# Optimization experiments

Measured on AMD Instinct MI355X. Metric: run time of the kernel, lower is better.

Reference implementation:

```python
import jax, jax.numpy as jnp
import numpy as np

B, T, D = 4, 2048, 1024

def layer_norm(x, gamma, bias):
    # NOTE: faithfully reproduces the source's (buggy) LN: x - mu/sqrt(var), unbiased var
    mu = jnp.mean(x, axis=-1, keepdims=True)
    var = jnp.var(x, axis=-1, ddof=1, keepdims=True)
    return (x - mu / jnp.sqrt(var)) * gamma + bias

def setup_inputs() -> dict:
    key = jax.random.key(0)
    ks = jax.random.split(key, 8)
    scale = 1.0 / np.sqrt(D)
    return {
        'x': jax.random.normal(ks[0], (B, T, D), dtype=jnp.float32),
        'gamma1': jnp.ones((D,), jnp.float32),
        'beta1': jnp.zeros((D,), jnp.float32),
        'w_q': jax.random.uniform(ks[1], (D, D), jnp.float32, -scale, scale),
        'w_k': jax.random.uniform(ks[2], (D, D), jnp.float32, -scale, scale),
        'w_v': jax.random.uniform(ks[3], (D, D), jnp.float32, -scale, scale),
        'gamma2': jnp.ones((D,), jnp.float32),
        'beta2': jnp.zeros((D,), jnp.float32),
        'W1': jax.random.uniform(ks[4], (D, D), jnp.float32, -scale, scale),
        'b1': jnp.zeros((D,), jnp.float32),
        'W2': jax.random.uniform(ks[5], (D, D), jnp.float32, -scale, scale),
        'b2': jnp.zeros((D,), jnp.float32),
    }

def reference(x, gamma1, beta1, w_q, w_k, w_v, gamma2, beta2, W1, b1, W2, b2):
    d_model = x.shape[-1]
    t = x.shape[1]
    h = layer_norm(x, gamma1, beta1)
    q = jnp.einsum('btk,kd->btd', h, w_q)
    k = jnp.einsum('btk,kd->btd', h, w_k)
    v = jnp.einsum('btk,kd->btd', h, w_v)
    scale = 1.0 / jnp.sqrt(jnp.asarray(d_model, x.dtype))
    causal = jnp.tril(jnp.ones((t, t), dtype=bool))
    mask = jnp.where(causal, 0.0, -jnp.inf).astype(x.dtype)
    scores = jnp.einsum('bqd,bkd->bqk', q, k) * scale + mask
    attn = jax.nn.softmax(scores, axis=-1)
    y = jnp.einsum('bqt,btd->bqd', attn, v) + x
    h2 = layer_norm(y, gamma2, beta2)
    out = jnp.maximum(h2 @ W1 + b1, 0.0) @ W2 + b2
    return out + y
```

## Files before the change

kernel.cpp:

```cpp
#include <hip/hip_runtime.h>
#include <hip/hip_bf16.h>
#include <math.h>

using bf16 = __hip_bfloat16;

static constexpr int Bn = 4;
static constexpr int Tn = 2048;
static constexpr int Dn = 1024;

typedef __attribute__((ext_vector_type(8))) short bf16x8;
typedef __attribute__((ext_vector_type(4))) float f32x4;

__device__ __forceinline__ float ldf(float v) { return v; }
__device__ __forceinline__ float ldf(bf16 v) { return __bfloat162float(v); }
__device__ __forceinline__ bf16 f2b(float v) { return __float2bfloat16(v); }
__device__ __forceinline__ float b2f(short s) {
    return __uint_as_float(((unsigned)(unsigned short)s) << 16);
}
__device__ __forceinline__ short f2bs(float v) {
    bf16 t = __float2bfloat16(v);
    return *reinterpret_cast<short*>(&t);
}

template <typename T> __device__ __forceinline__ T from_float(float v);
template <> __device__ __forceinline__ float from_float<float>(float v) { return v; }
template <> __device__ __forceinline__ bf16 from_float<bf16>(float v) { return f2b(v); }

__device__ __forceinline__ void load4(const float* p, float* v) {
    const float4 t = *(const float4*)p;
    v[0] = t.x; v[1] = t.y; v[2] = t.z; v[3] = t.w;
}
__device__ __forceinline__ void load4(const bf16* p, float* v) {
    const short4 t = *(const short4*)p;
    v[0] = b2f(t.x); v[1] = b2f(t.y); v[2] = b2f(t.z); v[3] = b2f(t.w);
}

__device__ __forceinline__ void async_copy16(const bf16* g, bf16* l) {
    __builtin_amdgcn_global_load_lds(
        (const __attribute__((address_space(1))) void*)g,
        (__attribute__((address_space(3))) void*)l,
        16, 0, 0);
}

template <int BN, int EPI, typename OutT, bool RELU>
__global__ __launch_bounds__(512, 2) void gemm8p(
    const bf16* __restrict__ A, const bf16* __restrict__ Bm,
    OutT* __restrict__ C, const float* __restrict__ bias,
    const bf16* __restrict__ res, bf16* __restrict__ vtp,
    int K, int lda, int ldb, int ldc)
{
    static_assert(EPI != 1 || BN == 128, "V-transpose epilogue needs BN=128");
    constexpr int BM = 256, BK = 32;
    constexpr int NT = BN / 64;
    constexpr int BUFE = (BM + BN) * BK;
    __shared__ __align__(16) bf16 smem[3 * BUFE];

    const int bm = blockIdx.x, bn = blockIdx.y;
    const int tid = threadIdx.x;
    const int wave = tid >> 6;
    const int lane = tid & 63;
    const int wm = wave >> 2;
    const int wn = wave & 3;
    const int lr = lane >> 2;
    const int lc = (lane & 3) * 8;
    const int arow = lane & 15;
    const int kq = (lane >> 4) * 8;

    const int NK = K / BK;

    const bf16* gA0 = A + (size_t)(bm * BM + wave * 16 + lr) * lda + lc;
    const bf16* gA1 = A + (size_t)(bm * BM + (wave + 8) * 16 + lr) * lda + lc;
    const bf16* gB0 = Bm + (size_t)(bn * BN + wave * 16 + lr) * ldb + lc;
    const bf16* gB1 = (BN == 256)
        ? Bm + (size_t)(bn * BN + (wave + 8) * 16 + lr) * ldb + lc : nullptr;

    f32x4 acc[8][NT] = {};

    {
        bf16* As0 = smem;
        bf16* Bs0 = smem + BM * BK;
        bf16* As1 = smem + BUFE;
        bf16* Bs1 = smem + BUFE + BM * BK;
        async_copy16(gA0, As0 + wave * 512);
        async_copy16(gA1, As0 + (wave + 8) * 512);
        async_copy16(gB0, Bs0 + wave * 512);
        if constexpr (BN == 256) async_copy16(gB1, Bs0 + (wave + 8) * 512);
        async_copy16(gA0 + BK, As1 + wave * 512);
        async_copy16(gA1 + BK, As1 + (wave + 8) * 512);
        async_copy16(gB0 + BK, Bs1 + wave * 512);
        if constexpr (BN == 256) async_copy16(gB1 + BK, Bs1 + (wave + 8) * 512);
    }
    if constexpr (BN == 256) asm volatile("s_waitcnt vmcnt(4)" ::: "memory");
    else                     asm volatile("s_waitcnt vmcnt(3)" ::: "memory");
    __builtin_amdgcn_s_barrier();

    int cb = 0;
    int sb = 2;
    for (int kt = 0; kt < NK; ++kt) {
        const bf16* As = smem + cb * BUFE;
        const bf16* Bs = As + BM * BK;
        const bool st = (kt + 2) < NK;
        const int koff = (kt + 2) * BK;

        bf16x8 af[8], bf0[NT / 2];
#pragma unroll
        for (int mt = 0; mt < 8; ++mt)
            af[mt] = *(const bf16x8*)&As[(wm * 8 + mt) * 512 + arow * 32 + kq];
#pragma unroll
        for (int nt = 0; nt < NT / 2; ++nt)
            bf0[nt] = *(const bf16x8*)&Bs[(wn * NT + nt) * 512 + arow * 32 + kq];
        if (st) {
            bf16* Ad = smem + sb * BUFE;
            async_copy16(gA0 + koff, Ad + wave * 512);
            async_copy16(gA1 + koff, Ad + (wave + 8) * 512);
        }
        __builtin_amdgcn_s_barrier();
        asm volatile("s_waitcnt lgkmcnt(0)" ::: "memory");
        __builtin_amdgcn_sched_barrier(0);
        __builtin_amdgcn_s_setprio(1);
#pragma unroll
        for (int mt = 0; mt < 8; ++mt)
#pragma unroll
            for (int nt = 0; nt < NT / 2; ++nt)
                acc[mt][nt] = __builtin_amdgcn_mfma_f32_16x16x32_bf16(
                    af[mt], bf0[nt], acc[mt][nt], 0, 0, 0);
        __builtin_amdgcn_s_setprio(0);
        __builtin_amdgcn_s_barrier();

        bf16x8 bf1[NT / 2];
#pragma unroll
        for (int nt = 0; nt < NT / 2; ++nt)
            bf1[nt] = *(const bf16x8*)&Bs[(wn * NT + NT / 2 + nt) * 512 + arow * 32 + kq];
        if (st) {
            bf16* Bd = smem + sb * BUFE + BM * BK;
            async_copy16(gB0 + koff, Bd + wave * 512);
            if constexpr (BN == 256) async_copy16(gB1 + koff, Bd + (wave + 8) * 512);
        }
        __builtin_amdgcn_s_barrier();
        asm volatile("s_waitcnt lgkmcnt(0)" ::: "memory");
        __builtin_amdgcn_sched_barrier(0);
        __builtin_amdgcn_s_setprio(1);
#pragma unroll
        for (int mt = 0; mt < 8; ++mt)
#pragma unroll
            for (int nt = 0; nt < NT / 2; ++nt)
                acc[mt][NT / 2 + nt] = __builtin_amdgcn_mfma_f32_16x16x32_bf16(
                    af[mt], bf1[nt], acc[mt][NT / 2 + nt], 0, 0, 0);
        __builtin_amdgcn_s_setprio(0);
        if (st) {
            if constexpr (BN == 256) asm volatile("s_waitcnt vmcnt(4)" ::: "memory");
            else                     asm volatile("s_waitcnt vmcnt(3)" ::: "memory");
        } else {
            asm volatile("s_waitcnt vmcnt(0)" ::: "memory");
        }
        __builtin_amdgcn_s_barrier();

        cb = (cb + 1 == 3) ? 0 : cb + 1;
        sb = (sb + 1 == 3) ? 0 : sb + 1;
    }

    const int qrow = (lane >> 4) * 4;
    const int ccol = lane & 15;

    if constexpr (EPI == 1) {
        bf16* tt = smem;
#pragma unroll
        for (int mt = 0; mt < 8; ++mt)
#pragma unroll
            for (int nt = 0; nt < NT; ++nt) {
                const int dl = wn * (NT * 16) + nt * 16 + ccol;
                const int tl = wm * 128 + mt * 16 + qrow;
                short4 o;
                o.x = f2bs(acc[mt][nt][0]);
                o.y = f2bs(acc[mt][nt][1]);
                o.z = f2bs(acc[mt][nt][2]);
                o.w = f2bs(acc[mt][nt][3]);
                *(short4*)&tt[dl * 264 + tl] = o;
            }
        __syncthreads();
        const int b = (bm * BM) >> 11;
        const int tin = (bm * BM) & (Tn - 1);
        const int dr = tid >> 4;
        const int t0 = (tid & 15) * 16;
#pragma unroll
        for (int p = 0; p < 4; ++p) {
            const int d = p * 32 + dr;
            const bf16* srcl = &tt[d * 264 + t0];
            bf16* dst = vtp + ((size_t)b * Dn + bn * BN + d) * Tn + tin + t0;
            ((bf16x8*)dst)[0] = ((const bf16x8*)srcl)[0];
            ((bf16x8*)dst)[1] = ((const bf16x8*)srcl)[1];
        }
        return;
    }

    const int row0 = bm * BM + wm * 128;
    const int col0 = bn * BN + wn * (NT * 16);
#pragma unroll
    for (int mt = 0; mt < 8; ++mt)
#pragma unroll
        for (int nt = 0; nt < NT; ++nt) {
            const int cc = col0 + nt * 16 + ccol;
            const float bv = bias ? bias[cc] : 0.0f;
#pragma unroll
            for (int r = 0; r < 4; ++r) {
                const int rr = row0 + mt * 16 + qrow + r;
                float v = acc[mt][nt][r] + bv;
                if (RELU) v = fmaxf(v, 0.0f);
                if (res) v += b2f(*(const short*)&res[(size_t)rr * ldc + cc]);
                C[(size_t)rr * ldc + cc] = from_float<OutT>(v);
            }
        }
}

template <int BM, int BN, int MINW, int EPI, typename OutT, typename ResT, bool RELU>
__global__ __launch_bounds__(256, MINW) void gemm_nt(
    const bf16* __restrict__ A, const bf16* __restrict__ Bm,
    OutT* __restrict__ C, const float* __restrict__ bias,
    const ResT* __restrict__ res, bf16* __restrict__ vtp,
    float* __restrict__ rowsum,
    int M, int N, int K, int lda, int ldb, int ldc,
    long sA, long sB, long sC, long sR, int mode)
{
    const int bm = blockIdx.x, bn = blockIdx.y, bz = blockIdx.z;
    if (mode == 1 && bn * BN > bm * BM + (BM - 1)) return;
    const int kend = bm * BM + BM;
    const int kmax = (mode == 2) ? (kend < K ? kend : K) : K;

    const bf16* Ab = A + (size_t)bz * sA;
    const bf16* Bb = Bm + (size_t)bz * sB;

    constexpr int WROWS = BM / 64;
    constexpr int WCOLS = 4 / WROWS;
    constexpr int TM = 64;
    constexpr int TN = BN / WCOLS;
    constexpr int MT = TM / 16;
    constexpr int NT = TN / 16;
    constexpr int nA = BM / 16;
    constexpr int nB = BN / 16;
    constexpr int STAGE = 2 * (BM + BN) * 32;

    __shared__ __align__(16) bf16 smem[STAGE];
    bf16* As = smem;
    bf16* Bs = smem + 2 * BM * 32;

    const int tid = threadIdx.x;
    const int wave = tid >> 6;
    const int lane = tid & 63;
    const int wm = wave / WCOLS;
    const int wn = wave % WCOLS;

    f32x4 acc[MT][NT] = {};

    const int lr = lane >> 2;
    const int lc = (lane & 3) * 8;
    const bf16* gAc[nA / 4]; bf16* lAc[nA / 4];
    const bf16* gBc[nB / 4]; bf16* lBc[nB / 4];
#pragma unroll
    for (int i = 0; i < nA / 4; ++i) {
        const int c = wave + 4 * i;
        gAc[i] = Ab + (size_t)(bm * BM + c * 16 + lr) * lda + lc;
        lAc[i] = &As[c * 512];
    }
#pragma unroll
    for (int i = 0; i < nB / 4; ++i) {
        const int c = wave + 4 * i;
        gBc[i] = Bb + (size_t)(bn * BN + c * 16 + lr) * ldb + lc;
        lBc[i] = &Bs[c * 512];
    }

    const int arow = lane & 15;
    const int kq = (lane >> 4) * 8;

    for (int k0 = 0; k0 < kmax; k0 += 64) {
#pragma unroll
        for (int hh = 0; hh < 2; ++hh) {
#pragma unroll
            for (int i = 0; i < nA / 4; ++i)
                async_copy16(gAc[i] + k0 + 32 * hh, lAc[i] + hh * (BM * 32));
#pragma unroll
            for (int i = 0; i < nB / 4; ++i)
                async_copy16(gBc[i] + k0 + 32 * hh, lBc[i] + hh * (BN * 32));
        }
        __syncthreads();

#pragma unroll
        for (int hh = 0; hh < 2; ++hh) {
            const bf16* Ah = As + hh * (BM * 32);
            const bf16* Bh = Bs + hh * (BN * 32);
            bf16x8 af[MT], bfm[NT];
#pragma unroll
            for (int t = 0; t < MT; ++t)
                af[t] = *(const bf16x8*)&Ah[(wm * TM + t * 16 + arow) * 32 + kq];
#pragma unroll
            for (int t = 0; t < NT; ++t)
                bfm[t] = *(const bf16x8*)&Bh[(wn * TN + t * 16 + arow) * 32 + kq];
#pragma unroll
            for (int mt = 0; mt < MT; ++mt)
#pragma unroll
                for (int nt = 0; nt < NT; ++nt)
                    acc[mt][nt] = __builtin_amdgcn_mfma_f32_16x16x32_bf16(
                        af[mt], bfm[nt], acc[mt][nt], 0, 0, 0);
        }
        __syncthreads();
    }

    const int rowBase = bm * BM + wm * TM;
    const int colBase = bn * BN + wn * TN;
    const int qrow = (lane >> 4) * 4;
    const int ccol = lane & 15;

    if (EPI == 2) {
        OutT* Cb = C + (size_t)bz * sC;
        float* rsb = rowsum + (size_t)bz * Tn;
        const float scale = 0.03125f;
#pragma unroll
        for (int mt = 0; mt < MT; ++mt) {
            float rsv[4] = {0.f, 0.f, 0.f, 0.f};
#pragma unroll
            for (int nt = 0; nt < NT; ++nt) {
                const int cc = colBase + nt * 16 + ccol;
#pragma unroll
                for (int r = 0; r < 4; ++r) {
                    const int rr = rowBase + mt * 16 + qrow + r;
                    float e = 0.0f;
                    if (cc <= rr) {
                        const short es = f2bs(__expf(acc[mt][nt][r] * scale));
                        Cb[(size_t)rr * ldc + cc] = *(const bf16*)&es;
                        e = b2f(es);
                    } else {
                        Cb[(size_t)rr * ldc + cc] = from_float<OutT>(0.0f);
                    }
                    rsv[r] += e;
                }
            }
#pragma unroll
            for (int r = 0; r < 4; ++r) {
                float v = rsv[r];
                v += __shfl_xor(v, 1);
                v += __shfl_xor(v, 2);
                v += __shfl_xor(v, 4);
                v += __shfl_xor(v, 8);
                if (ccol == 0)
                    atomicAdd(rsb + rowBase + mt * 16 + qrow + r, v);
            }
        }
        return;
    }

    OutT* Cb = C + (size_t)bz * sC;
    const ResT* Rb = res ? (res + (size_t)bz * sR) : nullptr;
    const float* rsb = (EPI == 3) ? (rowsum + (size_t)bz * Tn) : nullptr;
#pragma unroll
    for (int mt = 0; mt < MT; ++mt) {
        float inv4[4];
        if (EPI == 3) {
#pragma unroll
            for (int r = 0; r < 4; ++r)
                inv4[r] = 1.0f / rsb[rowBase + mt * 16 + qrow + r];
        }
#pragma unroll
        for (int nt = 0; nt < NT; ++nt) {
            const int cc = colBase + nt * 16 + ccol;
            const float bv = bias ? bias[cc] : 0.0f;
#pragma unroll
            for (int r = 0; r < 4; ++r) {
                const int rr = rowBase + mt * 16 + qrow + r;
                float v = acc[mt][nt][r];
                if (EPI == 3) v *= inv4[r];
                v += bv;
                if (RELU) v = fmaxf(v, 0.0f);
                if (Rb) v += ldf(Rb[(size_t)rr * ldc + cc]);
                Cb[(size_t)rr * ldc + cc] = from_float<OutT>(v);
            }
        }
    }
}

template <typename InT>
__device__ __forceinline__ void ln_row(
    const InT* __restrict__ xr, const float* __restrict__ gamma,
    const float* __restrict__ beta, bf16* __restrict__ orow, int tid)
{
    const int j = tid * 4;
    float v[4];
    load4(xr + j, v);
    float s = v[0] + v[1] + v[2] + v[3];
    float sq = v[0] * v[0] + v[1] * v[1] + v[2] * v[2] + v[3] * v[3];
#pragma unroll
    for (int o = 32; o > 0; o >>= 1) {
        s += __shfl_down(s, o);
        sq += __shfl_down(sq, o);
    }
    __shared__ float red[2][4];
    const int lane = tid & 63, w = tid >> 6;
    if (lane == 0) { red[0][w] = s; red[1][w] = sq; }
    __syncthreads();
    s  = red[0][0] + red[0][1] + red[0][2] + red[0][3];
    sq = red[1][0] + red[1][1] + red[1][2] + red[1][3];
    const float mean = s / (float)Dn;
    const float var = (sq - s * s / (float)Dn) / (float)(Dn - 1);
    const float coef = mean * rsqrtf(var);

    const float4 g = *(const float4*)(gamma + j);
    const float4 be = *(const float4*)(beta + j);
    short4 o;
    o.x = f2bs((v[0] - coef) * g.x + be.x);
    o.y = f2bs((v[1] - coef) * g.y + be.y);
    o.z = f2bs((v[2] - coef) * g.z + be.z);
    o.w = f2bs((v[3] - coef) * g.w + be.w);
    *(short4*)(orow + j) = o;
}

template <typename InT>
__global__ __launch_bounds__(256) void ln_kernel(
    const InT* __restrict__ x, const float* __restrict__ gamma,
    const float* __restrict__ beta, bf16* __restrict__ out)
{
    const int row = blockIdx.x;
    ln_row(x + (size_t)row * Dn, gamma, beta, out + (size_t)row * Dn, threadIdx.x);
}

struct WPtrs { const float* p[5]; };

__global__ __launch_bounds__(256) void prep_kernel(
    WPtrs wp, bf16* __restrict__ wdst, float* __restrict__ rowsum,
    const float* __restrict__ x, const float* __restrict__ gamma1,
    const float* __restrict__ beta1, bf16* __restrict__ h)
{
    const int bx = blockIdx.x;
    if (bx < 5120) {
        __shared__ bf16 tile[32][33];
        const int z = bx >> 10;
        const int t = bx & 1023;
        const float* src = wp.p[z];
        bf16* d = wdst + (size_t)z * Dn * Dn;
        const int c0 = (t & 31) * 32, r0 = (t >> 5) * 32;
        const int tx = threadIdx.x & 31;
        const int ty = threadIdx.x >> 5;
#pragma unroll
        for (int dy = 0; dy < 32; dy += 8)
            tile[ty + dy][tx] = f2b(src[(size_t)(r0 + ty + dy) * Dn + (c0 + tx)]);
        __syncthreads();
#pragma unroll
        for (int dy = 0; dy < 32; dy += 8)
            d[(size_t)(c0 + ty + dy) * Dn + (r0 + tx)] = tile[tx][ty + dy];
    } else if (bx < 5128) {
        const int base = (bx - 5120) * 1024;
#pragma unroll
        for (int i = 0; i < 4; ++i) rowsum[base + i * 256 + threadIdx.x] = 0.0f;
    } else {
        const int row = bx - 5128;
        ln_row(x + (size_t)row * Dn, gamma1, beta1, h + (size_t)row * Dn, threadIdx.x);
    }
}

extern "C" void kernel_launch(void* const* d_in, const int* in_sizes, int n_in,
                              void* d_out, int out_size, void* d_ws, size_t ws_size,
                              hipStream_t stream) {
    const float* x      = (const float*)d_in[0];
    const float* gamma1 = (const float*)d_in[1];
    const float* beta1  = (const float*)d_in[2];
    const float* w_q    = (const float*)d_in[3];
    const float* w_k    = (const float*)d_in[4];
    const float* w_v    = (const float*)d_in[5];
    const float* gamma2 = (const float*)d_in[6];
    const float* beta2  = (const float*)d_in[7];
    const float* W1     = (const float*)d_in[8];
    const float* b1     = (const float*)d_in[9];
    const float* W2     = (const float*)d_in[10];
    const float* b2     = (const float*)d_in[11];
    float* out = (float*)d_out;

    char* ws = (char*)d_ws;
    size_t off = 0;
    auto alloc = [&](size_t bytes) {
        char* p = ws + off;
        off += (bytes + 255) & ~(size_t)255;
        return p;
    };
    const size_t BT = (size_t)Bn * Tn;
    bf16* h    = (bf16*)alloc(BT * Dn * 2);
    bf16* qk   = (bf16*)alloc(BT * 2 * Dn * 2);
    bf16* vt   = (bf16*)alloc(BT * Dn * 2);
    bf16* wbuf = (bf16*)alloc((size_t)5 * Dn * Dn * 2);
    bf16* S    = (bf16*)alloc((size_t)Bn * Tn * Tn * 2);
    bf16* y    = (bf16*)alloc(BT * Dn * 2);
    float* rowsum = (float*)alloc((size_t)Bn * Tn * 4);
    bf16* h2   = h;
    bf16* mid  = qk;

    const dim3 blk(256);
    const long TD  = (long)Tn * Dn;
    const long TT  = (long)Tn * Tn;
    const long TD2 = (long)Tn * 2 * Dn;

    WPtrs wp; wp.p[0] = w_q; wp.p[1] = w_k; wp.p[2] = w_v; wp.p[3] = W1; wp.p[4] = W2;
    prep_kernel<<<dim3(5128 + (unsigned)BT, 1, 1), blk, 0, stream>>>(
        wp, wbuf, rowsum, x, gamma1, beta1, h);

    gemm8p<256, 0, bf16, false><<<dim3(32, 8, 1), dim3(512), 0, stream>>>(
        h, wbuf, qk, nullptr, nullptr, nullptr, Dn, Dn, Dn, 2 * Dn);

    gemm8p<128, 1, bf16, false><<<dim3(32, 8, 1), dim3(512), 0, stream>>>(
        h, wbuf + (size_t)2 * Dn * Dn, (bf16*)nullptr, nullptr, nullptr, vt,
        Dn, Dn, Dn, 0);

    gemm_nt<128, 128, 4, 2, bf16, float, false><<<dim3(16, 16, Bn), blk, 0, stream>>>(
        qk, qk + 1024, S, nullptr, nullptr, nullptr, rowsum,
        Tn, Tn, Dn, 2 * Dn, 2 * Dn, Tn, TD2, TD2, TT, 0, 1);

    gemm_nt<128, 128, 4, 3, bf16, float, false><<<dim3(16, 8, Bn), blk, 0, stream>>>(
        S, vt, y, nullptr, x, nullptr, rowsum,
        Tn, Dn, Tn, Tn, Tn, Dn, TT, TD, TD, TD, 2);

    ln_kernel<bf16><<<dim3((unsigned)BT), blk, 0, stream>>>(y, gamma2, beta2, h2);

    gemm8p<128, 0, bf16, true><<<dim3(32, 8, 1), dim3(512), 0, stream>>>(
        h2, wbuf + (size_t)3 * Dn * Dn, mid, b1, nullptr, nullptr,
        Dn, Dn, Dn, Dn);

    gemm8p<128, 0, float, false><<<dim3(32, 8, 1), dim3(512), 0, stream>>>(
        mid, wbuf + (size_t)4 * Dn * Dn, out, b2, y, nullptr,
        Dn, Dn, Dn, Dn);
}
```

Before: 362.5 us.

## Reorder attention GEMM grids to launch heavy causal rows first; use gemm_nt for FFN

The QK^T and PV GEMM grids are rearranged so that blockIdx.z maps to reversed row tiles, which launches the longest causal-masked row blocks first. The goal is better load balance, since the PV K-loop length grows with the row index. The two FFN GEMMs move from the 512-thread gemm8p kernel to the 256-thread gemm_nt kernel with 128x128 tiles. The unused vtp parameter is dropped and the mode numbers are remapped.

```diff
diff --git a/kernel.cpp b/kernel.cpp
--- a/kernel.cpp
+++ b/kernel.cpp
@@ -216,15 +216,20 @@
 __global__ __launch_bounds__(256, MINW) void gemm_nt(
     const bf16* __restrict__ A, const bf16* __restrict__ Bm,
     OutT* __restrict__ C, const float* __restrict__ bias,
-    const ResT* __restrict__ res, bf16* __restrict__ vtp,
-    float* __restrict__ rowsum,
+    const ResT* __restrict__ res, float* __restrict__ rowsum,
     int M, int N, int K, int lda, int ldb, int ldc,
     long sA, long sB, long sC, long sR, int mode)
 {
-    const int bm = blockIdx.x, bn = blockIdx.y, bz = blockIdx.z;
-    if (mode == 1 && bn * BN > bm * BM + (BM - 1)) return;
+    int bm, bn, bz;
+    if (mode >= 3) {
+        bn = blockIdx.x; bz = blockIdx.y;
+        bm = (int)gridDim.z - 1 - (int)blockIdx.z;
+    } else {
+        bm = blockIdx.x; bn = blockIdx.y; bz = blockIdx.z;
+    }
+    if (mode == 4 && bn * BN > bm * BM + (BM - 1)) return;
     const int kend = bm * BM + BM;
-    const int kmax = (mode == 2) ? (kend < K ? kend : K) : K;
+    const int kmax = (mode == 3) ? (kend < K ? kend : K) : K;
 
     const bf16* Ab = A + (size_t)bz * sA;
     const bf16* Bb = Bm + (size_t)bz * sB;
@@ -490,36 +495,38 @@
     bf16* mid  = qk;
 
     const dim3 blk(256);
+    const dim3 blk512(512);
     const long TD  = (long)Tn * Dn;
     const long TT  = (long)Tn * Tn;
     const long TD2 = (long)Tn * 2 * Dn;
+    const size_t DD = (size_t)Dn * Dn;
 
     WPtrs wp; wp.p[0] = w_q; wp.p[1] = w_k; wp.p[2] = w_v; wp.p[3] = W1; wp.p[4] = W2;
     prep_kernel<<<dim3(5128 + (unsigned)BT, 1, 1), blk, 0, stream>>>(
         wp, wbuf, rowsum, x, gamma1, beta1, h);
 
-    gemm8p<256, 0, bf16, false><<<dim3(32, 8, 1), dim3(512), 0, stream>>>(
+    gemm8p<256, 0, bf16, false><<<dim3(32, 8, 1), blk512, 0, stream>>>(
         h, wbuf, qk, nullptr, nullptr, nullptr, Dn, Dn, Dn, 2 * Dn);
 
-    gemm8p<128, 1, bf16, false><<<dim3(32, 8, 1), dim3(512), 0, stream>>>(
-        h, wbuf + (size_t)2 * Dn * Dn, (bf16*)nullptr, nullptr, nullptr, vt,
+    gemm8p<128, 1, bf16, false><<<dim3(32, 8, 1), blk512, 0, stream>>>(
+        h, wbuf + 2 * DD, (bf16*)nullptr, nullptr, nullptr, vt,
         Dn, Dn, Dn, 0);
 
-    gemm_nt<128, 128, 4, 2, bf16, float, false><<<dim3(16, 16, Bn), blk, 0, stream>>>(
-        qk, qk + 1024, S, nullptr, nullptr, nullptr, rowsum,
-        Tn, Tn, Dn, 2 * Dn, 2 * Dn, Tn, TD2, TD2, TT, 0, 1);
-
-    gemm_nt<128, 128, 4, 3, bf16, float, false><<<dim3(16, 8, Bn), blk, 0, stream>>>(
-        S, vt, y, nullptr, x, nullptr, rowsum,
-        Tn, Dn, Tn, Tn, Tn, Dn, TT, TD, TD, TD, 2);
+    gemm_nt<128, 128, 4, 2, bf16, float, false><<<dim3(16, Bn, 16), blk, 0, stream>>>(
+        qk, qk + 1024, S, nullptr, nullptr, rowsum,
+        Tn, Tn, Dn, 2 * Dn, 2 * Dn, Tn, TD2, TD2, TT, 0, 4);
+
+    gemm_nt<128, 128, 4, 3, bf16, float, false><<<dim3(8, Bn, 16), blk, 0, stream>>>(
+        S, vt, y, nullptr, x, rowsum,
+        Tn, Dn, Tn, Tn, Tn, Dn, TT, TD, TD, TD, 3);
 
     ln_kernel<bf16><<<dim3((unsigned)BT), blk, 0, stream>>>(y, gamma2, beta2, h2);
 
-    gemm8p<128, 0, bf16, true><<<dim3(32, 8, 1), dim3(512), 0, stream>>>(
-        h2, wbuf + (size_t)3 * Dn * Dn, mid, b1, nullptr, nullptr,
-        Dn, Dn, Dn, Dn);
-
-    gemm8p<128, 0, float, false><<<dim3(32, 8, 1), dim3(512), 0, stream>>>(
-        mid, wbuf + (size_t)4 * Dn * Dn, out, b2, y, nullptr,
-        Dn, Dn, Dn, Dn);
-}
+    gemm_nt<128, 128, 4, 0, bf16, float, true><<<dim3(64, 8, 1), blk, 0, stream>>>(
+        h2, wbuf + 3 * DD, mid, b1, nullptr, nullptr,
+        (int)BT, Dn, Dn, Dn, Dn, Dn, 0, 0, 0, 0, 0);
+
+    gemm_nt<128, 128, 4, 0, float, bf16, false><<<dim3(64, 8, 1), blk, 0, stream>>>(
+        mid, wbuf + 4 * DD, out, b2, y, nullptr,
+        (int)BT, Dn, Dn, Dn, Dn, Dn, 0, 0, 0, 0, 0);
+}
```

Measured after the change: 351.4 us. 3.1% less time.
